# Kernel optimization log

Hardware: AMD Instinct MI355X
Metric: run time of the kernel (lower is better)

Reference implementation:

```python
import jax, jax.numpy as jnp
import numpy as np

N_NODES = 50000
N_EDGES = 800000
D_IN = 64
D_HID = 64
D_OUT = 64


def setup_inputs() -> dict:
    key = jax.random.key(0)
    ks = jax.random.split(key, 10)
    x = jax.random.normal(ks[0], (N_NODES, D_IN), dtype=jnp.float32)
    src = jax.random.randint(ks[1], (N_EDGES,), 0, N_NODES, dtype=jnp.int32)
    dst = jax.random.randint(ks[2], (N_EDGES,), 0, N_NODES, dtype=jnp.int32)
    s = 1.0 / np.sqrt(D_IN)
    W0 = jax.random.uniform(ks[3], (D_IN, D_HID), jnp.float32, -s, s)
    b0 = jnp.zeros((D_HID,), jnp.float32)
    W1 = jax.random.uniform(ks[4], (D_HID, D_HID), jnp.float32, -s, s)
    b1 = jnp.zeros((D_HID,), jnp.float32)
    W2 = jax.random.uniform(ks[5], (D_HID, D_OUT), jnp.float32, -s, s)
    b2 = jnp.zeros((D_OUT,), jnp.float32)
    return {"x": x, "src": src, "dst": dst, "W0": W0, "b0": b0,
            "W1": W1, "b1": b1, "W2": W2, "b2": b2}


def reference(x, src, dst, W0, b0, W1, b1, W2, b2):
    N = x.shape[0]
    # in-degree (constant across layers)
    deg = jax.ops.segment_sum(jnp.ones(src.shape[0], x.dtype), dst, num_segments=N)
    inv = (1.0 / (deg + 1.0))[:, None]  # [N,1] gcn normalizer (deg + self)

    def sage_gcn(h, W, b):
        # gather neighbor feats along edges, scatter-add to destinations
        agg = jax.ops.segment_sum(h[src], dst, num_segments=N)  # [N,d]
        h_neigh = (agg + h) * inv
        return h_neigh @ W + b

    h = sage_gcn(x, W0, b0)
    h = jax.nn.relu(h)
    h = sage_gcn(h, W1, b1)
    h = jax.nn.relu(h)
    h = sage_gcn(h, W2, b2)
    return h
```

## Files before the change

kernel.cpp:

```cpp
#include <hip/hip_runtime.h>

#define D 64

__global__ void count_deg_kernel(const int* __restrict__ dst, int* __restrict__ deg, int nE) {
    int e4 = (blockIdx.x * blockDim.x + threadIdx.x) * 4;
    if (e4 + 3 < nE) {
        int4 d = *(const int4*)(dst + e4);
        atomicAdd(&deg[d.x], 1);
        atomicAdd(&deg[d.y], 1);
        atomicAdd(&deg[d.z], 1);
        atomicAdd(&deg[d.w], 1);
    } else {
        for (int e = e4; e < nE; ++e) atomicAdd(&deg[dst[e]], 1);
    }
}

__global__ __launch_bounds__(256) void scan_a_kernel(const int* __restrict__ deg,
                                                     int* __restrict__ row_ptr,
                                                     int* __restrict__ blocksums, int N) {
    __shared__ int s[256];
    int t = threadIdx.x;
    int i = blockIdx.x * 256 + t;
    int v = (i < N) ? deg[i] : 0;
    s[t] = v;
    __syncthreads();
    #pragma unroll
    for (int d = 1; d < 256; d <<= 1) {
        int u = (t >= d) ? s[t - d] : 0;
        __syncthreads();
        s[t] += u;
        __syncthreads();
    }
    if (i < N) row_ptr[i] = s[t] - v;
    if (t == 255) blocksums[blockIdx.x] = s[255];
}

__global__ __launch_bounds__(256) void scan_b_kernel(int* __restrict__ blocksums,
                                                     int* __restrict__ row_ptr,
                                                     int nb, int N) {
    __shared__ int s[256];
    int t = threadIdx.x;
    int v = (t < nb) ? blocksums[t] : 0;
    s[t] = v;
    __syncthreads();
    #pragma unroll
    for (int d = 1; d < 256; d <<= 1) {
        int u = (t >= d) ? s[t - d] : 0;
        __syncthreads();
        s[t] += u;
        __syncthreads();
    }
    if (t < nb) blocksums[t] = s[t] - v;
    if (t == 255) row_ptr[N] = s[255];
}

__global__ __launch_bounds__(256) void scan_c_kernel(int* __restrict__ row_ptr,
                                                     int* __restrict__ cursor,
                                                     const int* __restrict__ blocksums, int N) {
    int i = blockIdx.x * 256 + threadIdx.x;
    if (i < N) {
        int r = row_ptr[i] + blocksums[blockIdx.x];
        row_ptr[i] = r;
        cursor[i] = r;
    }
}

__global__ __launch_bounds__(256) void fill_csr_sliced_kernel(
    const int* __restrict__ src, const int* __restrict__ dst,
    int* __restrict__ cursor, int* __restrict__ col,
    int nE, int slice_size)
{
    const int g  = blockIdx.x & 7;
    const int gb = blockIdx.x >> 3;
    const int lo = g * slice_size;
    const int hi = lo + slice_size;
    int e4 = (gb * 256 + (int)threadIdx.x) * 4;
    if (e4 + 3 < nE) {
        int4 d = *(const int4*)(dst + e4);
        bool m0 = (d.x >= lo) & (d.x < hi);
        bool m1 = (d.y >= lo) & (d.y < hi);
        bool m2 = (d.z >= lo) & (d.z < hi);
        bool m3 = (d.w >= lo) & (d.w < hi);
        if (m0 | m1 | m2 | m3) {
            int4 s = *(const int4*)(src + e4);
            if (m0) col[atomicAdd(&cursor[d.x], 1)] = s.x;
            if (m1) col[atomicAdd(&cursor[d.y], 1)] = s.y;
            if (m2) col[atomicAdd(&cursor[d.z], 1)] = s.z;
            if (m3) col[atomicAdd(&cursor[d.w], 1)] = s.w;
        }
    } else if (e4 < nE) {
        for (int e = e4; e < nE; ++e) {
            int dd = dst[e];
            if (dd >= lo && dd < hi) col[atomicAdd(&cursor[dd], 1)] = src[e];
        }
    }
}

__global__ __launch_bounds__(256, 4) void sage_layer_kernel(
    const float* __restrict__ h, const int* __restrict__ row_ptr,
    const int* __restrict__ col, const float* __restrict__ W,
    const float* __restrict__ bias, float* __restrict__ out,
    int N, int do_relu)
{
    const int lane = threadIdx.x & 63;
    const int sub  = lane >> 4;
    const int fq   = lane & 15;
    const int w    = threadIdx.x >> 6;

    float Wreg[D];
    #pragma unroll
    for (int k = 0; k < D; ++k) Wreg[k] = W[k * D + lane];
    const float bj = bias[lane];

    const float4* __restrict__ h4 = (const float4*)h;

    const int nwaves = gridDim.x * 4;
    for (int i0 = blockIdx.x * 4 + w; i0 < N; i0 += nwaves) {
        const int i   = __builtin_amdgcn_readfirstlane(i0);
        const int rs  = __builtin_amdgcn_readfirstlane(row_ptr[i]);
        const int re  = __builtin_amdgcn_readfirstlane(row_ptr[i + 1]);
        const int deg = re - rs;

        float4 a0 = {0,0,0,0}, a1 = {0,0,0,0}, a2 = {0,0,0,0}, a3 = {0,0,0,0};

        for (int e0 = rs; e0 < re; e0 += 64) {
            int ee = e0 + lane;
            int idxv = col[(ee < re) ? ee : (re - 1)];
            int rem = re - e0;
            int steps = (((rem < 64) ? rem : 64) + 3) >> 2;
            int t = 0;
            for (; t + 4 <= steps; t += 4) {
                int base = (t << 2) + sub;
                int s0 = __shfl(idxv, base);
                int s1 = __shfl(idxv, base + 4);
                int s2 = __shfl(idxv, base + 8);
                int s3 = __shfl(idxv, base + 12);
                float4 v0 = h4[(size_t)s0 * 16 + fq];
                float4 v1 = h4[(size_t)s1 * 16 + fq];
                float4 v2 = h4[(size_t)s2 * 16 + fq];
                float4 v3 = h4[(size_t)s3 * 16 + fq];
                a0.x += v0.x; a0.y += v0.y; a0.z += v0.z; a0.w += v0.w;
                a1.x += v1.x; a1.y += v1.y; a1.z += v1.z; a1.w += v1.w;
                a2.x += v2.x; a2.y += v2.y; a2.z += v2.z; a2.w += v2.w;
                a3.x += v3.x; a3.y += v3.y; a3.z += v3.z; a3.w += v3.w;
            }
            for (; t < steps; ++t) {
                int s0 = __shfl(idxv, (t << 2) + sub);
                float4 v0 = h4[(size_t)s0 * 16 + fq];
                a0.x += v0.x; a0.y += v0.y; a0.z += v0.z; a0.w += v0.w;
            }
        }

        float4 tt;
        tt.x = (a0.x + a1.x) + (a2.x + a3.x);
        tt.y = (a0.y + a1.y) + (a2.y + a3.y);
        tt.z = (a0.z + a1.z) + (a2.z + a3.z);
        tt.w = (a0.w + a1.w) + (a2.w + a3.w);
        tt.x += __shfl_xor(tt.x, 16); tt.x += __shfl_xor(tt.x, 32);
        tt.y += __shfl_xor(tt.y, 16); tt.y += __shfl_xor(tt.y, 32);
        tt.z += __shfl_xor(tt.z, 16); tt.z += __shfl_xor(tt.z, 32);
        tt.w += __shfl_xor(tt.w, 16); tt.w += __shfl_xor(tt.w, 32);

        int pad = (-deg) & 3;
        if (deg > 0 && pad) {
            int last = __builtin_amdgcn_readfirstlane(col[re - 1]);
            float4 vl = h4[(size_t)last * 16 + fq];
            float fp = (float)pad;
            tt.x = fmaf(-fp, vl.x, tt.x);
            tt.y = fmaf(-fp, vl.y, tt.y);
            tt.z = fmaf(-fp, vl.z, tt.z);
            tt.w = fmaf(-fp, vl.w, tt.w);
        }

        float4 hs = h4[(size_t)i * 16 + fq];
        float invd = 1.0f / (float)(deg + 1);
        tt.x = (tt.x + hs.x) * invd;
        tt.y = (tt.y + hs.y) * invd;
        tt.z = (tt.z + hs.z) * invd;
        tt.w = (tt.w + hs.w) * invd;

        float o = bj;
        #pragma unroll
        for (int k = 0; k < D; ++k) {
            float comp = ((k & 3) == 0) ? tt.x : ((k & 3) == 1) ? tt.y
                       : ((k & 3) == 2) ? tt.z : tt.w;
            int ti = __builtin_amdgcn_readlane(__float_as_int(comp), k >> 2);
            o = fmaf(__int_as_float(ti), Wreg[k], o);
        }
        if (do_relu) o = fmaxf(o, 0.0f);
        out[(size_t)i * D + lane] = o;
    }
}

extern "C" void kernel_launch(void* const* d_in, const int* in_sizes, int n_in,
                              void* d_out, int out_size, void* d_ws, size_t ws_size,
                              hipStream_t stream) {
    const float* x   = (const float*)d_in[0];
    const int*   src = (const int*)d_in[1];
    const int*   dst = (const int*)d_in[2];
    const float* W0  = (const float*)d_in[3];
    const float* b0  = (const float*)d_in[4];
    const float* W1  = (const float*)d_in[5];
    const float* b1  = (const float*)d_in[6];
    const float* W2  = (const float*)d_in[7];
    const float* b2  = (const float*)d_in[8];
    float* out = (float*)d_out;

    const int N = in_sizes[0] / D;
    const int E = in_sizes[1];

    const int scan_blocks = (N + 255) / 256;

    char* ws = (char*)d_ws;
    size_t off = 0;
    auto alloc = [&](size_t bytes) -> void* {
        void* p = ws + off;
        off = (off + bytes + 255) & ~(size_t)255;
        return p;
    };
    int*   deg       = (int*)  alloc((size_t)N * sizeof(int));
    int*   row_ptr   = (int*)  alloc((size_t)(N + 1) * sizeof(int));
    int*   cursor    = (int*)  alloc((size_t)N * sizeof(int));
    int*   blocksums = (int*)  alloc((size_t)scan_blocks * sizeof(int));
    int*   col       = (int*)  alloc((size_t)E * sizeof(int));
    float* h1        = (float*)alloc((size_t)N * D * sizeof(float));
    float* h2        = (float*)alloc((size_t)N * D * sizeof(float));

    hipMemsetAsync(deg, 0, (size_t)N * sizeof(int), stream);
    const int e4_blocks = (E / 4 + 255) / 256;
    count_deg_kernel<<<e4_blocks, 256, 0, stream>>>(dst, deg, E);
    scan_a_kernel<<<scan_blocks, 256, 0, stream>>>(deg, row_ptr, blocksums, N);
    scan_b_kernel<<<1, 256, 0, stream>>>(blocksums, row_ptr, scan_blocks, N);
    scan_c_kernel<<<scan_blocks, 256, 0, stream>>>(row_ptr, cursor, blocksums, N);
    const int slice_size = (N + 7) / 8;
    fill_csr_sliced_kernel<<<e4_blocks * 8, 256, 0, stream>>>(src, dst, cursor, col, E, slice_size);

    const int layer_blocks = 4096;

    sage_layer_kernel<<<layer_blocks, 256, 0, stream>>>(x,  row_ptr, col, W0, b0, h1,  N, 1);
    sage_layer_kernel<<<layer_blocks, 256, 0, stream>>>(h1, row_ptr, col, W1, b1, h2,  N, 1);
    sage_layer_kernel<<<layer_blocks, 256, 0, stream>>>(h2, row_ptr, col, W2, b2, out, N, 0);
}
```

Baseline: 289.0 us.

## Stage W in LDS, prefetch next node's CSR row, and raise occupancy

New measurement: 655.6 us. 2.27x slower.

```diff
diff --git a/kernel.cpp b/kernel.cpp
--- a/kernel.cpp
+++ b/kernel.cpp
@@ -96,66 +96,105 @@
     }
 }
 
-__global__ __launch_bounds__(256, 4) void sage_layer_kernel(
+__global__ __launch_bounds__(256, 8) void sage_layer_kernel(
     const float* __restrict__ h, const int* __restrict__ row_ptr,
     const int* __restrict__ col, const float* __restrict__ W,
     const float* __restrict__ bias, float* __restrict__ out,
     int N, int do_relu)
 {
+    __shared__ float Wlds[D * D];
+    {
+        const float4* W4 = (const float4*)W;
+        float4* Wl4 = (float4*)Wlds;
+        #pragma unroll
+        for (int t = 0; t < 4; ++t)
+            Wl4[t * 256 + threadIdx.x] = W4[t * 256 + threadIdx.x];
+    }
+    __syncthreads();
+
     const int lane = threadIdx.x & 63;
     const int sub  = lane >> 4;
     const int fq   = lane & 15;
     const int w    = threadIdx.x >> 6;
-
-    float Wreg[D];
-    #pragma unroll
-    for (int k = 0; k < D; ++k) Wreg[k] = W[k * D + lane];
     const float bj = bias[lane];
-
     const float4* __restrict__ h4 = (const float4*)h;
-
     const int nwaves = gridDim.x * 4;
-    for (int i0 = blockIdx.x * 4 + w; i0 < N; i0 += nwaves) {
-        const int i   = __builtin_amdgcn_readfirstlane(i0);
-        const int rs  = __builtin_amdgcn_readfirstlane(row_ptr[i]);
-        const int re  = __builtin_amdgcn_readfirstlane(row_ptr[i + 1]);
+
+    int i = blockIdx.x * 4 + w;
+    if (i >= N) return;
+
+    int rs = __builtin_amdgcn_readfirstlane(row_ptr[i]);
+    int re = __builtin_amdgcn_readfirstlane(row_ptr[i + 1]);
+    {
+        int ee = rs + lane;
+        int cl = (ee < re) ? ee : ((re > rs) ? re - 1 : rs);
+    }
+    int ee0 = rs + lane;
+    int idxv = __builtin_nontemporal_load(&col[(ee0 < re) ? ee0 : ((re > rs) ? re - 1 : rs)]);
+
+    while (true) {
+        const int i_next = i + nwaves;
+
+        int rpA = 0, rpB = 0;
+        if (i_next < N) {
+            rpA = row_ptr[i_next];
+            rpB = row_ptr[i_next + 1];
+        }
+        float4 hs = h4[(size_t)i * 16 + fq];
+
         const int deg = re - rs;
-
-        float4 a0 = {0,0,0,0}, a1 = {0,0,0,0}, a2 = {0,0,0,0}, a3 = {0,0,0,0};
-
-        for (int e0 = rs; e0 < re; e0 += 64) {
-            int ee = e0 + lane;
-            int idxv = col[(ee < re) ? ee : (re - 1)];
-            int rem = re - e0;
+        float4 a0 = {0,0,0,0}, a1 = {0,0,0,0};
+        int last_iv = idxv;
+
+        auto gather_chunk = [&](int iv, int rem) {
             int steps = (((rem < 64) ? rem : 64) + 3) >> 2;
             int t = 0;
             for (; t + 4 <= steps; t += 4) {
                 int base = (t << 2) + sub;
-                int s0 = __shfl(idxv, base);
-                int s1 = __shfl(idxv, base + 4);
-                int s2 = __shfl(idxv, base + 8);
-                int s3 = __shfl(idxv, base + 12);
+                int s0 = __shfl(iv, base);
+                int s1 = __shfl(iv, base + 4);
+                int s2 = __shfl(iv, base + 8);
+                int s3 = __shfl(iv, base + 12);
                 float4 v0 = h4[(size_t)s0 * 16 + fq];
                 float4 v1 = h4[(size_t)s1 * 16 + fq];
                 float4 v2 = h4[(size_t)s2 * 16 + fq];
                 float4 v3 = h4[(size_t)s3 * 16 + fq];
                 a0.x += v0.x; a0.y += v0.y; a0.z += v0.z; a0.w += v0.w;
                 a1.x += v1.x; a1.y += v1.y; a1.z += v1.z; a1.w += v1.w;
-                a2.x += v2.x; a2.y += v2.y; a2.z += v2.z; a2.w += v2.w;
-                a3.x += v3.x; a3.y += v3.y; a3.z += v3.z; a3.w += v3.w;
+                a0.x += v2.x; a0.y += v2.y; a0.z += v2.z; a0.w += v2.w;
+                a1.x += v3.x; a1.y += v3.y; a1.z += v3.z; a1.w += v3.w;
             }
             for (; t < steps; ++t) {
-                int s0 = __shfl(idxv, (t << 2) + sub);
+                int s0 = __shfl(iv, (t << 2) + sub);
                 float4 v0 = h4[(size_t)s0 * 16 + fq];
                 a0.x += v0.x; a0.y += v0.y; a0.z += v0.z; a0.w += v0.w;
             }
+        };
+
+        if (deg > 0) {
+            gather_chunk(idxv, deg);
+            for (int e0 = rs + 64; e0 < re; e0 += 64) {
+                int e1 = e0 + lane;
+                int iv = __builtin_nontemporal_load(&col[(e1 < re) ? e1 : re - 1]);
+                last_iv = iv;
+                gather_chunk(iv, re - e0);
+            }
+        }
+
+        int rs2 = 0, re2 = 0, idxv2 = 0;
+        if (i_next < N) {
+            rs2 = __builtin_amdgcn_readfirstlane(rpA);
+            re2 = __builtin_amdgcn_readfirstlane(rpB);
+            int e2 = rs2 + lane;
+            int cl = (e2 < re2) ? e2 : ((re2 > rs2) ? re2 - 1 : rs2);
+            idxv2 = __builtin_nontemporal_load(&col[cl]);
         }
 
         float4 tt;
-        tt.x = (a0.x + a1.x) + (a2.x + a3.x);
-        tt.y = (a0.y + a1.y) + (a2.y + a3.y);
-        tt.z = (a0.z + a1.z) + (a2.z + a3.z);
-        tt.w = (a0.w + a1.w) + (a2.w + a3.w);
+        tt.x = a0.x + a1.x;
+        tt.y = a0.y + a1.y;
+        tt.z = a0.z + a1.z;
+        tt.w = a0.w + a1.w;
         tt.x += __shfl_xor(tt.x, 16); tt.x += __shfl_xor(tt.x, 32);
         tt.y += __shfl_xor(tt.y, 16); tt.y += __shfl_xor(tt.y, 32);
         tt.z += __shfl_xor(tt.z, 16); tt.z += __shfl_xor(tt.z, 32);
@@ -163,7 +202,7 @@
 
         int pad = (-deg) & 3;
         if (deg > 0 && pad) {
-            int last = __builtin_amdgcn_readfirstlane(col[re - 1]);
+            int last = __shfl(last_iv, 63);
             float4 vl = h4[(size_t)last * 16 + fq];
             float fp = (float)pad;
             tt.x = fmaf(-fp, vl.x, tt.x);
@@ -172,23 +211,31 @@
             tt.w = fmaf(-fp, vl.w, tt.w);
         }
 
-        float4 hs = h4[(size_t)i * 16 + fq];
         float invd = 1.0f / (float)(deg + 1);
         tt.x = (tt.x + hs.x) * invd;
         tt.y = (tt.y + hs.y) * invd;
         tt.z = (tt.z + hs.z) * invd;
         tt.w = (tt.w + hs.w) * invd;
 
-        float o = bj;
+        float o0 = bj, o1 = 0.0f, o2 = 0.0f, o3 = 0.0f;
         #pragma unroll
-        for (int k = 0; k < D; ++k) {
-            float comp = ((k & 3) == 0) ? tt.x : ((k & 3) == 1) ? tt.y
-                       : ((k & 3) == 2) ? tt.z : tt.w;
-            int ti = __builtin_amdgcn_readlane(__float_as_int(comp), k >> 2);
-            o = fmaf(__int_as_float(ti), Wreg[k], o);
-        }
+        for (int k = 0; k < D; k += 4) {
+            const int q = k >> 2;
+            int t0 = __builtin_amdgcn_readlane(__float_as_int(tt.x), q);
+            int t1 = __builtin_amdgcn_readlane(__float_as_int(tt.y), q);
+            int t2 = __builtin_amdgcn_readlane(__float_as_int(tt.z), q);
+            int t3 = __builtin_amdgcn_readlane(__float_as_int(tt.w), q);
+            o0 = fmaf(__int_as_float(t0), Wlds[(k + 0) * D + lane], o0);
+            o1 = fmaf(__int_as_float(t1), Wlds[(k + 1) * D + lane], o1);
+            o2 = fmaf(__int_as_float(t2), Wlds[(k + 2) * D + lane], o2);
+            o3 = fmaf(__int_as_float(t3), Wlds[(k + 3) * D + lane], o3);
+        }
+        float o = (o0 + o1) + (o2 + o3);
         if (do_relu) o = fmaxf(o, 0.0f);
-        out[(size_t)i * D + lane] = o;
+        __builtin_nontemporal_store(o, &out[(size_t)i * D + lane]);
+
+        if (i_next >= N) break;
+        i = i_next; rs = rs2; re = re2; idxv = idxv2;
     }
 }
 
@@ -222,7 +269,7 @@
     int*   row_ptr   = (int*)  alloc((size_t)(N + 1) * sizeof(int));
     int*   cursor    = (int*)  alloc((size_t)N * sizeof(int));
     int*   blocksums = (int*)  alloc((size_t)scan_blocks * sizeof(int));
-    int*   col       = (int*)  alloc((size_t)E * sizeof(int));
+    int*   col       = (int*)  alloc((size_t)(E + 64) * sizeof(int));
     float* h1        = (float*)alloc((size_t)N * D * sizeof(float));
     float* h2        = (float*)alloc((size_t)N * D * sizeof(float));
 
```
